# Kernel optimization log

Measured on AMD Instinct MI355X. Metric: run time of the kernel, lower is better.

The kernel has to match this reference:

```python
import jax, jax.numpy as jnp
import numpy as np

B, N, C, H, DEPTH = 64, 256, 384, 8, 6
HD = C // H  # 48
SCALE = HD ** -0.5
LN_EPS = 1e-5


def setup_inputs() -> dict:
    key = jax.random.key(0)
    ks = jax.random.split(key, 12)
    g = lambda k, shape, s=0.05: jax.random.normal(k, shape, jnp.float32) * s
    return {
        "x": jax.random.normal(ks[0], (B, N, 2), jnp.float32),
        "mask": jnp.zeros((B, N), jnp.float32),  # additive padding mask (0 = keep)
        "emb_w1": g(ks[1], (C, 2), 0.5),
        "emb_b1": jnp.zeros((C,), jnp.float32),
        "emb_w2": g(ks[2], (C, C)),
        "emb_b2": jnp.zeros((C,), jnp.float32),
        "qkv_w": g(ks[3], (DEPTH, 3 * C, C)),
        "proj_w": g(ks[4], (DEPTH, C, C)),
        "proj_b": jnp.zeros((DEPTH, C), jnp.float32),
        "mlp_w1": g(ks[5], (DEPTH, C, C)),
        "mlp_b1": jnp.zeros((DEPTH, C), jnp.float32),
        "mlp_w2": g(ks[6], (DEPTH, C, C)),
        "mlp_b2": jnp.zeros((DEPTH, C), jnp.float32),
        "ln1_s": jnp.ones((DEPTH, C), jnp.float32),
        "ln1_b": jnp.zeros((DEPTH, C), jnp.float32),
        "ln2_s": jnp.ones((DEPTH, C), jnp.float32),
        "ln2_b": jnp.zeros((DEPTH, C), jnp.float32),
    }


def _layernorm(x, s, b):
    mu = jnp.mean(x, axis=-1, keepdims=True)
    var = jnp.mean((x - mu) ** 2, axis=-1, keepdims=True)
    return (x - mu) * jax.lax.rsqrt(var + LN_EPS) * s + b


def _rope(t):
    # t: (B, H, N, HD); interleaved rotary, matching the torch module
    hd = t.shape[-1]
    inv_freq = 1.0 / (10000.0 ** (jnp.arange(0, hd, 2, dtype=jnp.float32) / hd))
    pos = jnp.arange(t.shape[2], dtype=jnp.float32)
    f = pos[:, None] * inv_freq[None, :]            # (N, HD/2)
    cos, sin = jnp.cos(f), jnp.sin(f)
    xu, xe = t[..., 0::2], t[..., 1::2]
    ru = xu * cos - xe * sin
    re = xu * sin + xe * cos
    return jnp.stack([ru, re], axis=-1).reshape(t.shape)


def reference(x, mask, emb_w1, emb_b1, emb_w2, emb_b2, qkv_w, proj_w, proj_b,
              mlp_w1, mlp_b1, mlp_w2, mlp_b2, ln1_s, ln1_b, ln2_s, ln2_b):
    # BallEmbedding: Linear -> ReLU -> Linear
    h = jax.nn.relu(x @ emb_w1.T + emb_b1) @ emb_w2.T + emb_b2  # (B, N, C)
    for i in range(DEPTH):
        # pre-norm rotary attention
        y = _layernorm(h, ln1_s[i], ln1_b[i])
        qkv = (y @ qkv_w[i].T).reshape(B, N, 3, H, HD).transpose(2, 0, 3, 1, 4)
        q, k, v = qkv[0], qkv[1], qkv[2]                      # (B, H, N, HD)
        q = _rope(q) * SCALE
        k = _rope(k)
        attn = jnp.einsum('bhqd,bhkd->bhqk', q, k)
        attn = attn + mask[:, None, None, :] + mask[:, None, :, None]
        attn = jax.nn.softmax(attn, axis=-1)
        o = jnp.einsum('bhqk,bhkd->bhqd', attn, v)
        o = o.transpose(0, 2, 1, 3).reshape(B, N, C)
        h = h + (o @ proj_w[i].T + proj_b[i])
        # pre-norm MLP (hidden = dim, ReLU)
        y = _layernorm(h, ln2_s[i], ln2_b[i])
        m = jax.nn.relu(y @ mlp_w1[i].T + mlp_b1[i]) @ mlp_w2[i].T + mlp_b2[i]
        h = h + m
    return h
```

## Files before the change

kernel.cpp:

```cpp
#include <hip/hip_runtime.h>
#include <hip/hip_bf16.h>
#include <math.h>

#define BATCH 64
#define SEQ   256
#define CH    384
#define NHEAD 8
#define HD    48
#define DEPTH 6
#define NTOK  (BATCH*SEQ)
#define C3    (3*CH)
#define LN_EPS 1e-5f
#define ATT_SCALE 0.14433756729740643f

typedef __attribute__((ext_vector_type(8)))  short bf16x8;
typedef __attribute__((ext_vector_type(4)))  float f32x4;
typedef __attribute__((ext_vector_type(16))) float f32x16;

__device__ __forceinline__ ushort f2bf(float f) {
    __hip_bfloat16 h = __float2bfloat16(f);
    return *(ushort*)&h;
}
__device__ __forceinline__ float bfu2f(ushort u) {
    uint t = ((uint)u) << 16;
    union { uint u; float f; } c; c.u = t; return c.f;
}
__device__ __forceinline__ uint pk2(float a, float b) {
    return (uint)f2bf(a) | ((uint)f2bf(b) << 16);
}

#define AS1(p) ((const __attribute__((address_space(1))) void*)(p))
#define AS3(p) ((__attribute__((address_space(3))) void*)(uintptr_t)(p))
#define WAITVMC(N) asm volatile("s_waitcnt vmcnt(" #N ")" ::: "memory")
#define TAILSYNC() do { \
    asm volatile("s_waitcnt lgkmcnt(0)" ::: "memory"); \
    __builtin_amdgcn_sched_barrier(0); \
    __builtin_amdgcn_s_barrier(); } while (0)

__global__ void init_kernel(float4* __restrict__ sb, float2* __restrict__ tbl) {
    int bid = blockIdx.x;
    if (bid < 384) {
        sb[bid*256 + threadIdx.x] = float4{0.f,0.f,0.f,0.f};
    } else {
        int pos = threadIdx.x;
        for (int j = 0; j < 24; ++j) {
            float freq = exp2f(-(float)j * (13.287712379549449f / 24.0f));
            float ang = (float)pos * freq;
            float s, c;
            sincosf(ang, &s, &c);
            tbl[pos*24 + j] = make_float2(c, s);
        }
    }
}

__global__ void f2bf3_kernel(const float* __restrict__ s0, const float* __restrict__ s1,
                             const float* __restrict__ s2, ushort* __restrict__ dst) {
    int bid = blockIdx.x;
    const float* src;
    int loc;
    if (bid < 144)      { src = s0; loc = bid; }
    else if (bid < 1008){ src = s1; loc = bid - 144; }
    else                { src = s2; loc = bid - 1008; }
    int li = loc*1024 + threadIdx.x*4;
    float4 v = *(const float4*)(src + li);
    ushort4 o;
    o.x = f2bf(v.x); o.y = f2bf(v.y); o.z = f2bf(v.z); o.w = f2bf(v.w);
    *(ushort4*)(dst + (size_t)bid*1024 + threadIdx.x*4) = o;
}

__global__ void embed1_kernel(const float* __restrict__ x, const float* __restrict__ w1,
                              const float* __restrict__ b1, ushort* __restrict__ out) {
    int idx = blockIdx.x*256 + threadIdx.x;
    int m = idx / CH, c = idx - m*CH;
    float v = x[m*2]*w1[c*2] + x[m*2+1]*w1[c*2+1] + b1[c];
    out[idx] = f2bf(fmaxf(v, 0.f));
}

__global__ __launch_bounds__(256) void prep_kernel(
        const float* __restrict__ Wsrc, const float* __restrict__ gam,
        const float* __restrict__ bet, const float* __restrict__ bias,
        int npl, ushort* __restrict__ Wdst, float2* __restrict__ uvout) {
    int rr   = blockIdx.x*4 + (threadIdx.x >> 6);
    int lane = threadIdx.x & 63;
    int layer = rr / npl;
    const float* wp = Wsrc + (size_t)rr*CH;
    const float* gp = gam + layer*CH;
    const float* bp = bet + layer*CH;
    float u = 0.f, vv = 0.f;
    if (lane < 48) {
        int c0 = lane*8;
        float w8[8];
        *(float4*)&w8[0] = *(const float4*)(wp + c0);
        *(float4*)&w8[4] = *(const float4*)(wp + c0 + 4);
        union { ushort us[8]; bf16x8 v; } o;
        #pragma unroll
        for (int j = 0; j < 8; ++j) {
            float wg = w8[j] * gp[c0+j];
            u  += wg;
            vv += bp[c0+j] * w8[j];
            o.us[j] = f2bf(wg);
        }
        *(bf16x8*)(Wdst + (size_t)rr*CH + c0) = o.v;
    }
    #pragma unroll
    for (int o = 1; o < 64; o <<= 1) { u += __shfl_xor(u, o); vv += __shfl_xor(vv, o); }
    if (lane == 0) {
        if (bias) vv += bias[rr];
        uvout[rr] = make_float2(u, vv);
    }
}

template<bool LNAFF, bool RELU, bool RESID, bool QKV>
__global__ __launch_bounds__(256) void gemm_kernel(
        const ushort* __restrict__ A,
        const ushort* __restrict__ W,
        const float*  __restrict__ bias,
        const float2* __restrict__ uv,
        const float2* __restrict__ sbr,
        const float*  __restrict__ resid,
        float*  __restrict__ hout,
        ushort* __restrict__ bout,
        int ldo, int nx,
        float2* __restrict__ sbw,
        ushort* __restrict__ vtbuf,
        const float2* __restrict__ tbl) {
    __shared__ __align__(16) ushort As[2][4096];
    __shared__ __align__(16) ushort Bs[2][8192];
    const int tid  = threadIdx.x;
    const int lane = tid & 63;
    const int w    = tid >> 6;
    const int l15  = lane & 15;
    const int g    = lane >> 4;
    const int wr   = (w >> 1) * 32;
    const int wc   = (w & 1) * 64;
    const int lin  = blockIdx.x;
    const int swz  = (lin & 7)*((int)gridDim.x >> 3) + (lin >> 3);
    const int m0   = (swz / nx) * 64;
    const int n0   = (swz % nx) * 128;

    const int srow = lane >> 3;
    const int scol = ((lane & 7) ^ srow) * 8;
    auto stage = [&](int pb, int t) {
        int k0 = t*64;
        #pragma unroll
        for (int c = 0; c < 6; ++c) {
            int chunk = w + c*4;
            if (chunk < 8) {
                const ushort* gp = A + (size_t)(m0 + chunk*8 + srow)*CH + k0 + scol;
                __builtin_amdgcn_global_load_lds(AS1(gp), AS3(&As[pb][chunk*512]), 16, 0, 0);
            } else {
                const ushort* gp = W + (size_t)(n0 + (chunk-8)*8 + srow)*CH + k0 + scol;
                __builtin_amdgcn_global_load_lds(AS1(gp), AS3(&Bs[pb][(chunk-8)*512]), 16, 0, 0);
            }
        }
    };

    f32x4 acc[2][4] = {};
    const int xm = (l15 & 7) << 4;

    stage(0, 0);
    for (int t = 0; t < 6; ++t) {
        if (t + 1 < 6) stage((t+1)&1, t+1);
        if (t < 5) { WAITVMC(6); } else { WAITVMC(0); }
        __builtin_amdgcn_s_barrier();
        const int pb = t & 1;
        #pragma unroll
        for (int kk = 0; kk < 2; ++kk) {
            bf16x8 a[2], b[4];
            #pragma unroll
            for (int i = 0; i < 2; ++i)
                a[i] = *(const bf16x8*)((const char*)As[pb]
                        + (wr + i*16 + l15)*128 + ((kk*64 + 16*g) ^ xm));
            #pragma unroll
            for (int j = 0; j < 4; ++j)
                b[j] = *(const bf16x8*)((const char*)Bs[pb]
                        + (wc + j*16 + l15)*128 + ((kk*64 + 16*g) ^ xm));
            #pragma unroll
            for (int i = 0; i < 2; ++i)
                #pragma unroll
                for (int j = 0; j < 4; ++j)
                    acc[i][j] = __builtin_amdgcn_mfma_f32_16x16x32_bf16(a[i], b[j], acc[i][j], 0, 0, 0);
        }
        TAILSYNC();
    }

    const int cbase = n0 + wc + l15;
    const int rbase = m0 + wr + g*4;
    if (LNAFF) {
        float2 uvv[4];
        #pragma unroll
        for (int j = 0; j < 4; ++j) uvv[j] = uv[cbase + j*16];
        const int region = QKV ? (n0 / 384) : 0;
        int hj[4], dj[4], jp[4];
        if (QKV) {
            #pragma unroll
            for (int j = 0; j < 4; ++j) {
                int nn = cbase + j*16 - region*384;
                if (region == 2) { hj[j] = nn / HD; dj[j] = nn - hj[j]*HD; }
                else             { jp[j] = (nn % HD) >> 1; }
            }
        }
        #pragma unroll
        for (int i = 0; i < 2; ++i) {
            float muv[4], invv[4];
            #pragma unroll
            for (int r = 0; r < 4; ++r) {
                float2 s2 = sbr[rbase + i*16 + r];
                float mu = s2.x * (1.0f/CH);
                float var = s2.y * (1.0f/CH) - mu*mu;
                muv[r] = mu; invv[r] = rsqrtf(var + LN_EPS);
            }
            if (QKV && region == 2) {
                int bb   = rbase >> 8;
                int seq0 = (rbase + i*16) & 255;
                #pragma unroll
                for (int j = 0; j < 4; ++j) {
                    float vr[4];
                    #pragma unroll
                    for (int r = 0; r < 4; ++r)
                        vr[r] = invv[r]*(acc[i][j][r] - muv[r]*uvv[j].x) + uvv[j].y;
                    uint2 val;
                    val.x = pk2(vr[0], vr[1]);
                    val.y = pk2(vr[2], vr[3]);
                    *(uint2*)(vtbuf + (((size_t)bb*NHEAD + hj[j])*64 + dj[j])*SEQ + seq0) = val;
                }
            } else {
                #pragma unroll
                for (int r = 0; r < 4; ++r) {
                    int m = rbase + i*16 + r;
                    int pos = m & 255;
                    #pragma unroll
                    for (int j = 0; j < 4; ++j) {
                        float v = invv[r]*(acc[i][j][r] - muv[r]*uvv[j].x) + uvv[j].y;
                        if (QKV) {
                            float vx = __shfl_xor(v, 1);
                            float2 cs = tbl[pos*24 + jp[j]];
                            v = (l15 & 1) ? (vx*cs.y + v*cs.x) : (v*cs.x - vx*cs.y);
                            if (region == 0) v *= ATT_SCALE;
                        }
                        if (RELU) v = fmaxf(v, 0.f);
                        bout[(size_t)m*ldo + cbase + j*16] = f2bf(v);
                    }
                }
            }
        }
    } else {
        float bj[4];
        #pragma unroll
        for (int j = 0; j < 4; ++j) bj[j] = bias[cbase + j*16];
        #pragma unroll
        for (int i = 0; i < 2; ++i)
            #pragma unroll
            for (int r = 0; r < 4; ++r) {
                int m = rbase + i*16 + r;
                #pragma unroll
                for (int j = 0; j < 4; ++j) {
                    int n = cbase + j*16;
                    float v = acc[i][j][r] + bj[j];
                    if (RESID) v += resid[(size_t)m*CH + n];
                    acc[i][j][r] = v;
                    hout[(size_t)m*CH + n] = v;
                    bout[(size_t)m*CH + n] = f2bf(v);
                }
            }
        if (sbw) {
            #pragma unroll
            for (int i = 0; i < 2; ++i)
                #pragma unroll
                for (int r = 0; r < 4; ++r) {
                    float s = 0.f, q = 0.f;
                    #pragma unroll
                    for (int j = 0; j < 4; ++j) {
                        float v = acc[i][j][r];
                        s += v; q += v*v;
                    }
                    #pragma unroll
                    for (int off = 1; off < 16; off <<= 1) {
                        s += __shfl_xor(s, off);
                        q += __shfl_xor(q, off);
                    }
                    if (l15 == 0) {
                        int m = rbase + i*16 + r;
                        atomicAdd(&sbw[m].x, s);
                        atomicAdd(&sbw[m].y, q);
                    }
                }
        }
    }
}

__global__ __launch_bounds__(512) void attn_kernel(
        const ushort* __restrict__ qkv, const ushort* __restrict__ vtbuf,
        const float* __restrict__ mask, ushort* __restrict__ obuf) {
    __shared__ __align__(16) ushort Kf[8*3*64*8];
    __shared__ __align__(16) ushort Vf[2*16*64*8];
    __shared__ float Ms[SEQ];

    const int bid = blockIdx.x;
    const int b   = bid >> 3;
    const int hh  = bid & 7;
    const int tid = threadIdx.x;
    const int lane = tid & 63;
    const int hi   = (lane >> 5);
    const int q5   = lane & 31;
    const int twv  = tid >> 6;
    const ushort* base = qkv + (size_t)b*SEQ*C3;

    {
        int row = twv*32 + q5;
        const ushort* kp = base + (size_t)row*C3 + CH + hh*HD + hi*8;
        #pragma unroll
        for (int s = 0; s < 3; ++s)
            __builtin_amdgcn_global_load_lds(AS1(kp + s*16), AS3(&Kf[(twv*3+s)*512]), 16, 0, 0);
    }
    {
        const ushort* vt = vtbuf + (size_t)(b*NHEAD + hh)*64*SEQ;
        #pragma unroll
        for (int p = 0; p < 4; ++p) {
            int dt = p >> 1;
            int sp = twv*2 + (p & 1);
            int dd = dt*32 + q5;
            const ushort* vp = vt + (size_t)dd*SEQ + sp*16 + hi*8;
            __builtin_amdgcn_global_load_lds(AS1(vp), AS3(&Vf[(dt*16+sp)*512]), 16, 0, 0);
        }
    }
    if (tid < SEQ) Ms[tid] = mask[b*SEQ + tid];

    const int qrow = twv*32 + q5;
    bf16x8 qf[3];
    {
        const ushort* qp = base + (size_t)qrow*C3 + hh*HD + hi*8;
        #pragma unroll
        for (int s = 0; s < 3; ++s) qf[s] = *(const bf16x8*)(qp + s*16);
    }
    __syncthreads();

    f32x16 st[8] = {};
    #pragma unroll
    for (int t = 0; t < 8; ++t)
        #pragma unroll
        for (int s = 0; s < 3; ++s) {
            bf16x8 af = *(const bf16x8*)&Kf[((t*3 + s)*64 + lane)*8];
            st[t] = __builtin_amdgcn_mfma_f32_32x32x16_bf16(af, qf[s], st[t], 0, 0, 0);
        }

    float mx = -1e30f;
    #pragma unroll
    for (int t = 0; t < 8; ++t)
        #pragma unroll
        for (int r = 0; r < 16; ++r) {
            int kt = t*32 + (r & 3) + 8*(r >> 2) + 4*hi;
            float s = st[t][r] + Ms[kt];
            st[t][r] = s;
            mx = fmaxf(mx, s);
        }
    mx = fmaxf(mx, __shfl_xor(mx, 32));
    float sum = 0.f;
    #pragma unroll
    for (int t = 0; t < 8; ++t)
        #pragma unroll
        for (int r = 0; r < 16; ++r) {
            float p = __expf(st[t][r] - mx);
            st[t][r] = p;
            sum += p;
        }
    sum += __shfl_xor(sum, 32);

    f32x16 oacc[2] = {};
    #pragma unroll
    for (int t = 0; t < 8; ++t) {
        uint w[4][2];
        #pragma unroll
        for (int g = 0; g < 4; ++g) {
            w[g][0] = pk2(st[t][g*4+0], st[t][g*4+1]);
            w[g][1] = pk2(st[t][g*4+2], st[t][g*4+3]);
        }
        #pragma unroll
        for (int o = 0; o < 2; ++o) {
            uint x0 = __shfl_xor(hi ? w[2*o][0] : w[2*o+1][0], 32);
            uint x1 = __shfl_xor(hi ? w[2*o][1] : w[2*o+1][1], 32);
            union { uint w[4]; bf16x8 v; } pf;
            if (hi == 0) { pf.w[0] = w[2*o][0]; pf.w[1] = w[2*o][1]; pf.w[2] = x0; pf.w[3] = x1; }
            else         { pf.w[0] = x0; pf.w[1] = x1; pf.w[2] = w[2*o+1][0]; pf.w[3] = w[2*o+1][1]; }
            int sp = t*2 + o;
            #pragma unroll
            for (int dt = 0; dt < 2; ++dt) {
                bf16x8 vf = *(const bf16x8*)&Vf[((dt*16 + sp)*64 + lane)*8];
                oacc[dt] = __builtin_amdgcn_mfma_f32_32x32x16_bf16(vf, pf.v, oacc[dt], 0, 0, 0);
            }
        }
    }

    float inv = 1.f / sum;
    ushort* op = obuf + ((size_t)(b*SEQ + qrow))*CH + hh*HD;
    #pragma unroll
    for (int dt = 0; dt < 2; ++dt)
        #pragma unroll
        for (int rg = 0; rg < 4; ++rg) {
            int d0 = dt*32 + rg*8 + hi*4;
            if (d0 < HD) {
                uint2 val;
                val.x = pk2(oacc[dt][rg*4+0]*inv, oacc[dt][rg*4+1]*inv);
                val.y = pk2(oacc[dt][rg*4+2]*inv, oacc[dt][rg*4+3]*inv);
                *(uint2*)(op + d0) = val;
            }
        }
}

extern "C" void kernel_launch(void* const* d_in, const int* in_sizes, int n_in,
                              void* d_out, int out_size, void* d_ws, size_t ws_size,
                              hipStream_t stream) {
    const float* x      = (const float*)d_in[0];
    const float* mask   = (const float*)d_in[1];
    const float* emb_w1 = (const float*)d_in[2];
    const float* emb_b1 = (const float*)d_in[3];
    const float* emb_w2 = (const float*)d_in[4];
    const float* emb_b2 = (const float*)d_in[5];
    const float* qkv_w  = (const float*)d_in[6];
    const float* proj_w = (const float*)d_in[7];
    const float* proj_b = (const float*)d_in[8];
    const float* mlp_w1 = (const float*)d_in[9];
    const float* mlp_b1 = (const float*)d_in[10];
    const float* mlp_w2 = (const float*)d_in[11];
    const float* mlp_b2 = (const float*)d_in[12];
    const float* ln1_s  = (const float*)d_in[13];
    const float* ln1_b  = (const float*)d_in[14];
    const float* ln2_s  = (const float*)d_in[15];
    const float* ln2_b  = (const float*)d_in[16];

    const size_t S1 = (size_t)NTOK*CH;
    float*  h     = (float*)d_ws;
    ushort* hbf   = (ushort*)(h + S1);
    ushort* qkvbf = hbf + S1;
    ushort* ybf   = qkvbf + 3*S1;
    ushort* t2bf  = ybf  + S1;
    ushort* obf   = t2bf + S1;
    ushort* vtbuf = obf  + S1;
    ushort* wb_emb2 = vtbuf + (size_t)BATCH*NHEAD*64*SEQ;
    ushort* wb_proj = wb_emb2 + 147456;
    ushort* wb_m2   = wb_proj + 884736;
    ushort* wqkvp   = wb_m2   + 884736;
    ushort* wm1p    = wqkvp   + 2654208;
    float2* uv_qkv  = (float2*)(wm1p + 884736);
    float2* uv_m1   = uv_qkv + 6912;
    float2* sb      = uv_m1  + 2304;
    float*  tbl     = (float*)(sb + 12*NTOK);
    const float2* tblc = (const float2*)tbl;

    init_kernel<<<385, 256, 0, stream>>>((float4*)sb, (float2*)tbl);
    f2bf3_kernel<<<1872, 256, 0, stream>>>(emb_w2, proj_w, mlp_w2, wb_emb2);
    prep_kernel<<<1728, 256, 0, stream>>>(qkv_w,  ln1_s, ln1_b, nullptr, C3, wqkvp, uv_qkv);
    prep_kernel<<<576,  256, 0, stream>>>(mlp_w1, ln2_s, ln2_b, mlp_b1,  CH, wm1p,  uv_m1);

    embed1_kernel<<<(NTOK*CH)/256, 256, 0, stream>>>(x, emb_w1, emb_b1, ybf);
    gemm_kernel<false,false,false,false><<<768, 256, 0, stream>>>(ybf, wb_emb2, emb_b2,
            nullptr, nullptr, nullptr, h, hbf, CH, 3, sb, nullptr, nullptr);

    for (int i = 0; i < DEPTH; ++i) {
        gemm_kernel<true,false,false,true><<<2304, 256, 0, stream>>>(hbf,
                wqkvp + (size_t)i*C3*CH, nullptr, uv_qkv + i*C3, sb + (size_t)(2*i)*NTOK,
                nullptr, nullptr, qkvbf, C3, 9, nullptr, vtbuf, tblc);
        attn_kernel<<<BATCH*NHEAD, 512, 0, stream>>>(qkvbf, vtbuf, mask, obf);
        gemm_kernel<false,false,true,false><<<768, 256, 0, stream>>>(obf,
                wb_proj + (size_t)i*CH*CH, proj_b + i*CH, nullptr, nullptr,
                h, h, hbf, CH, 3, sb + (size_t)(2*i+1)*NTOK, nullptr, nullptr);
        gemm_kernel<true,true,false,false><<<768, 256, 0, stream>>>(hbf,
                wm1p + (size_t)i*CH*CH, nullptr, uv_m1 + i*CH, sb + (size_t)(2*i+1)*NTOK,
                nullptr, nullptr, t2bf, CH, 3, nullptr, nullptr, nullptr);
        gemm_kernel<false,false,true,false><<<768, 256, 0, stream>>>(t2bf,
                wb_m2 + (size_t)i*CH*CH, mlp_b2 + i*CH, nullptr, nullptr,
                h, h, hbf, CH, 3, (i < DEPTH-1) ? (sb + (size_t)(2*i+2)*NTOK) : nullptr,
                nullptr, nullptr);
    }
    hipMemcpyAsync(d_out, h, S1*sizeof(float), hipMemcpyDeviceToDevice, stream);
}
```

Measured before the change: 846.5 us.

## Triple-buffer GEMM staging and split attention softmax into two online groups

The GEMM kernel goes from a double-buffered to a triple-buffered LDS pipeline, prefetching two K-tiles ahead with adjusted vmcnt waits to hide more global-load latency, at the cost of 50% more shared memory per block. The attention kernel now processes keys in two groups of 128 with an online-softmax running max and sum, so only 4 score tiles are live at once instead of 8. This is meant to lower VGPR pressure and raise occupancy, in exchange for extra rescaling of the output accumulators and exp work.

Result: slower. 900.3 us (+6.4%).

```diff
diff --git a/kernel.cpp b/kernel.cpp
--- a/kernel.cpp
+++ b/kernel.cpp
@@ -124,8 +124,8 @@
         float2* __restrict__ sbw,
         ushort* __restrict__ vtbuf,
         const float2* __restrict__ tbl) {
-    __shared__ __align__(16) ushort As[2][4096];
-    __shared__ __align__(16) ushort Bs[2][8192];
+    __shared__ __align__(16) ushort As[3][4096];
+    __shared__ __align__(16) ushort Bs[3][8192];
     const int tid  = threadIdx.x;
     const int lane = tid & 63;
     const int w    = tid >> 6;
@@ -158,12 +158,12 @@
     f32x4 acc[2][4] = {};
     const int xm = (l15 & 7) << 4;
 
-    stage(0, 0);
+    stage(0, 0); stage(1, 1);
     for (int t = 0; t < 6; ++t) {
-        if (t + 1 < 6) stage((t+1)&1, t+1);
-        if (t < 5) { WAITVMC(6); } else { WAITVMC(0); }
+        if (t + 2 < 6) stage((t+2)%3, t+2);
+        if (t < 4) { WAITVMC(12); } else if (t == 4) { WAITVMC(6); } else { WAITVMC(0); }
         __builtin_amdgcn_s_barrier();
-        const int pb = t & 1;
+        const int pb = t % 3;
         #pragma unroll
         for (int kk = 0; kk < 2; ++kk) {
             bf16x8 a[2], b[4];
@@ -335,63 +335,77 @@
     }
     __syncthreads();
 
-    f32x16 st[8] = {};
+    float m_run = -1e30f, l_run = 0.f;
+    f32x16 oacc[2] = {};
+
     #pragma unroll
-    for (int t = 0; t < 8; ++t)
-        #pragma unroll
-        for (int s = 0; s < 3; ++s) {
-            bf16x8 af = *(const bf16x8*)&Kf[((t*3 + s)*64 + lane)*8];
-            st[t] = __builtin_amdgcn_mfma_f32_32x32x16_bf16(af, qf[s], st[t], 0, 0, 0);
-        }
-
-    float mx = -1e30f;
-    #pragma unroll
-    for (int t = 0; t < 8; ++t)
-        #pragma unroll
-        for (int r = 0; r < 16; ++r) {
-            int kt = t*32 + (r & 3) + 8*(r >> 2) + 4*hi;
-            float s = st[t][r] + Ms[kt];
-            st[t][r] = s;
-            mx = fmaxf(mx, s);
-        }
-    mx = fmaxf(mx, __shfl_xor(mx, 32));
-    float sum = 0.f;
-    #pragma unroll
-    for (int t = 0; t < 8; ++t)
-        #pragma unroll
-        for (int r = 0; r < 16; ++r) {
-            float p = __expf(st[t][r] - mx);
-            st[t][r] = p;
-            sum += p;
-        }
-    sum += __shfl_xor(sum, 32);
-
-    f32x16 oacc[2] = {};
-    #pragma unroll
-    for (int t = 0; t < 8; ++t) {
-        uint w[4][2];
-        #pragma unroll
-        for (int g = 0; g < 4; ++g) {
-            w[g][0] = pk2(st[t][g*4+0], st[t][g*4+1]);
-            w[g][1] = pk2(st[t][g*4+2], st[t][g*4+3]);
-        }
-        #pragma unroll
-        for (int o = 0; o < 2; ++o) {
-            uint x0 = __shfl_xor(hi ? w[2*o][0] : w[2*o+1][0], 32);
-            uint x1 = __shfl_xor(hi ? w[2*o][1] : w[2*o+1][1], 32);
-            union { uint w[4]; bf16x8 v; } pf;
-            if (hi == 0) { pf.w[0] = w[2*o][0]; pf.w[1] = w[2*o][1]; pf.w[2] = x0; pf.w[3] = x1; }
-            else         { pf.w[0] = x0; pf.w[1] = x1; pf.w[2] = w[2*o+1][0]; pf.w[3] = w[2*o+1][1]; }
-            int sp = t*2 + o;
-            #pragma unroll
-            for (int dt = 0; dt < 2; ++dt) {
-                bf16x8 vf = *(const bf16x8*)&Vf[((dt*16 + sp)*64 + lane)*8];
-                oacc[dt] = __builtin_amdgcn_mfma_f32_32x32x16_bf16(vf, pf.v, oacc[dt], 0, 0, 0);
-            }
-        }
-    }
-
-    float inv = 1.f / sum;
+    for (int grp = 0; grp < 2; ++grp) {
+        f32x16 st[4] = {};
+        #pragma unroll
+        for (int t4 = 0; t4 < 4; ++t4) {
+            int t = grp*4 + t4;
+            #pragma unroll
+            for (int s = 0; s < 3; ++s) {
+                bf16x8 af = *(const bf16x8*)&Kf[((t*3 + s)*64 + lane)*8];
+                st[t4] = __builtin_amdgcn_mfma_f32_32x32x16_bf16(af, qf[s], st[t4], 0, 0, 0);
+            }
+        }
+        float gm = -1e30f;
+        #pragma unroll
+        for (int t4 = 0; t4 < 4; ++t4)
+            #pragma unroll
+            for (int r = 0; r < 16; ++r) {
+                int kt = (grp*4 + t4)*32 + (r & 3) + 8*(r >> 2) + 4*hi;
+                float s = st[t4][r] + Ms[kt];
+                st[t4][r] = s;
+                gm = fmaxf(gm, s);
+            }
+        gm = fmaxf(gm, __shfl_xor(gm, 32));
+        float m_new = fmaxf(m_run, gm);
+        float corr = __expf(m_run - m_new);
+        l_run *= corr;
+        #pragma unroll
+        for (int dt = 0; dt < 2; ++dt)
+            #pragma unroll
+            for (int r = 0; r < 16; ++r) oacc[dt][r] *= corr;
+        float psum = 0.f;
+        #pragma unroll
+        for (int t4 = 0; t4 < 4; ++t4)
+            #pragma unroll
+            for (int r = 0; r < 16; ++r) {
+                float p = __expf(st[t4][r] - m_new);
+                st[t4][r] = p;
+                psum += p;
+            }
+        l_run += psum;
+        #pragma unroll
+        for (int t4 = 0; t4 < 4; ++t4) {
+            uint w[4][2];
+            #pragma unroll
+            for (int g = 0; g < 4; ++g) {
+                w[g][0] = pk2(st[t4][g*4+0], st[t4][g*4+1]);
+                w[g][1] = pk2(st[t4][g*4+2], st[t4][g*4+3]);
+            }
+            #pragma unroll
+            for (int o = 0; o < 2; ++o) {
+                uint x0 = __shfl_xor(hi ? w[2*o][0] : w[2*o+1][0], 32);
+                uint x1 = __shfl_xor(hi ? w[2*o][1] : w[2*o+1][1], 32);
+                union { uint w[4]; bf16x8 v; } pf;
+                if (hi == 0) { pf.w[0] = w[2*o][0]; pf.w[1] = w[2*o][1]; pf.w[2] = x0; pf.w[3] = x1; }
+                else         { pf.w[0] = x0; pf.w[1] = x1; pf.w[2] = w[2*o+1][0]; pf.w[3] = w[2*o+1][1]; }
+                int sp = (grp*4 + t4)*2 + o;
+                #pragma unroll
+                for (int dt = 0; dt < 2; ++dt) {
+                    bf16x8 vf = *(const bf16x8*)&Vf[((dt*16 + sp)*64 + lane)*8];
+                    oacc[dt] = __builtin_amdgcn_mfma_f32_32x32x16_bf16(vf, pf.v, oacc[dt], 0, 0, 0);
+                }
+            }
+        }
+        m_run = m_new;
+    }
+
+    float tot = l_run + __shfl_xor(l_run, 32);
+    float inv = 1.f / tot;
     ushort* op = obuf + ((size_t)(b*SEQ + qrow))*CH + hh*HD;
     #pragma unroll
     for (int dt = 0; dt < 2; ++dt)
```
